# Optimization experiments

Measured on AMD Instinct MI355X. Metric: run time of the kernel, lower is better.

## Reference

```python
import jax, jax.numpy as jnp
import numpy as np

K_DEPTH = 3
JAC_A = 1.0  # alpha (Jacobi a)
JAC_B = 1.0  # beta  (Jacobi b)


def jacobi_filter(sig, gammas):
    """Polynomial graph filter g(sigma) = sum_k gamma_k * P_k^{(a,b)}(sigma),
    Jacobi recurrence applied elementwise (Sigma is diagonal spectrum), domain [-1,1],
    fixed inner scalings (fixI=True => alphas=1)."""
    a, b = JAC_A, JAC_B
    xs = [jnp.ones_like(sig)]
    # L = 1
    coef1 = (a - b) / 2.0
    coef2 = (a + b + 2.0) / 2.0
    xs.append(coef1 * xs[0] + coef2 * sig * xs[0])
    for L in range(2, K_DEPTH + 1):
        cl = 2.0 * L * (L + a + b) * (2 * L - 2 + a + b)
        c1 = (2 * L + a + b - 1) * (2 * L + a + b) * (2 * L + a + b - 2)
        c2 = (2 * L + a + b - 1) * (a * a - b * b)
        c3 = 2.0 * (L - 1 + a) * (L - 1 + b) * (2 * L + a + b)
        xs.append((c1 / cl) * sig * xs[-1] - (c2 / cl) * xs[-1] - (c3 / cl) * xs[-2])
    basis = jnp.stack(xs, axis=0)  # [K+1, B, H, L, d]
    return jnp.einsum('k,kbhld->bhld', gammas, basis)


def setup_inputs() -> dict:
    key = jax.random.key(0)
    ks = jax.random.split(key, 7)
    B, L, Ha, Hs, d = 4, 2048, 4, 4, 64
    mk = lambda k, H: jax.random.normal(k, (B, L, H, d), dtype=jnp.float32)
    return {
        'U': mk(ks[0], Ha),
        'Sigma': mk(ks[1], Ha),
        'V': mk(ks[2], Ha),
        'values': mk(ks[3], Ha),
        'queries_softmax': mk(ks[4], Hs),
        'keys_softmax': mk(ks[5], Hs),
        'values_softmax': mk(ks[6], Hs),
        'gammas': jnp.ones((K_DEPTH + 1,), dtype=jnp.float32),
    }


def reference(U, Sigma, V, values, queries_softmax, keys_softmax, values_softmax, gammas):
    d_k = U.shape[-1]
    # ---- AGF (SVD) heads ----
    Uh = jax.nn.softmax(jnp.transpose(U, (0, 2, 1, 3)), axis=-1)        # [B,H,L,d]
    Vt = jax.nn.softmax(jnp.transpose(V, (0, 2, 3, 1)), axis=-1)        # [B,H,d,L]
    vals = jnp.transpose(values, (0, 2, 1, 3))                           # [B,H,L,d]
    sig = jax.nn.sigmoid(jnp.transpose(Sigma, (0, 2, 1, 3)))             # [B,H,L,d]
    gf = jacobi_filter(sig, gammas)                                       # [B,H,L,d]
    kv = jnp.einsum('bhdl,bhle->bhde', Vt, vals)                          # [B,H,d,d]
    out_agf = jnp.einsum('bhld,bhde->bhle', Uh * gf, kv)                  # [B,H,L,d]
    out_agf = jnp.transpose(out_agf, (0, 2, 1, 3))                        # [B,L,H,d]
    # ---- orthogonality loss ----
    eye = jnp.eye(d_k, dtype=Uh.dtype)
    sym_u = jnp.einsum('bhld,bhle->bhde', Uh, Uh) - eye
    sym_v = jnp.einsum('bhdl,bhel->bhde', Vt, Vt) - eye
    ortho_loss = jnp.mean(jnp.abs(sym_u), axis=(1, 2, 3)) + jnp.mean(jnp.abs(sym_v), axis=(1, 2, 3))
    # ---- softmax (flash) heads ----
    q = jnp.transpose(queries_softmax, (0, 2, 1, 3))
    k = jnp.transpose(keys_softmax, (0, 2, 1, 3))
    v = jnp.transpose(values_softmax, (0, 2, 1, 3))
    scores = jnp.einsum('bhld,bhsd->bhls', q, k) / jnp.sqrt(jnp.asarray(d_k, q.dtype))
    attn = jax.nn.softmax(scores, axis=-1)
    out_sm = jnp.einsum('bhls,bhsd->bhld', attn, v)
    out_sm = jnp.transpose(out_sm, (0, 2, 1, 3))                          # [B,L,H,d]
    out = jnp.concatenate([out_agf, out_sm], axis=2)                      # [B,L,2H,d]
    return out, ortho_loss
```

## Files before the change

### kernel.cpp

```cpp
#include <hip/hip_runtime.h>
#include <hip/hip_bf16.h>

#define BB 4
#define SEQ 2048
#define NH 4
#define D 64
#define NPAIR 16
#define HOUT 8
#define LOSS_BASE ((size_t)BB * SEQ * HOUT * D)

#define N_PART   (4 * 16 * 3 * 4096)
#define OFF_SPART N_PART
#define N_SPART  (16 * 32 * 64)
#define OFF_LPART (OFF_SPART + N_SPART)
#define N_LPART  (2 * 16 * 2048)
#define OFF_F32_END (OFF_LPART + N_LPART)
#define USZ ((size_t)16 * 2048 * 64)

typedef __attribute__((ext_vector_type(8))) short bf16x8;
typedef __attribute__((ext_vector_type(4))) float f32x4;
typedef __attribute__((ext_vector_type(8))) unsigned short us8;
typedef __attribute__((ext_vector_type(4))) unsigned short us4;

__device__ __forceinline__ unsigned short f2bf(float x) {
    union { float f; unsigned u; } v; v.f = x;
    unsigned r = v.u + 0x7fffu + ((v.u >> 16) & 1u);
    return (unsigned short)(r >> 16);
}
__device__ __forceinline__ float bf2f(unsigned short u) {
    union { unsigned u; float f; } v; v.u = ((unsigned)u) << 16; return v.f;
}
__device__ __forceinline__ void load16(const float* p, float* v) {
    const float4* q = (const float4*)p;
    float4 a = q[0], b = q[1], c = q[2], d = q[3];
    v[0]=a.x; v[1]=a.y; v[2]=a.z; v[3]=a.w;
    v[4]=b.x; v[5]=b.y; v[6]=b.z; v[7]=b.w;
    v[8]=c.x; v[9]=c.y; v[10]=c.z; v[11]=c.w;
    v[12]=d.x; v[13]=d.y; v[14]=d.z; v[15]=d.w;
}
__device__ __forceinline__ void wr_bf16x16(unsigned short* dst, const float* v) {
    us8 w0, w1;
#pragma unroll
    for (int i = 0; i < 8; i++) { w0[i] = f2bf(v[i]); w1[i] = f2bf(v[8 + i]); }
    *(us8*)dst = w0; *(us8*)(dst + 8) = w1;
}

__global__ __launch_bounds__(256) void prep(const float* __restrict__ U, const float* __restrict__ Sg,
                                            const float* __restrict__ Vagf, const float* __restrict__ vals,
                                            const float* __restrict__ Ksm, const float* __restrict__ Vsm,
                                            const float* __restrict__ gam,
                                            float* __restrict__ ws, unsigned short* __restrict__ usb,
                                            float* __restrict__ out) {
    int lt = blockIdx.x, p = blockIdx.y, stage = blockIdx.z;
    int b = p >> 2, h = p & 3;
    int tid = threadIdx.x;
    int r = tid >> 2;
    int c0 = (tid & 3) * 16;
    __shared__ float T[64][68];
    unsigned short* Khi   = usb;
    unsigned short* VbfT  = usb + USZ;
    unsigned short* UhT   = usb + 2 * USZ;
    unsigned short* EhiT  = usb + 3 * USZ;
    unsigned short* valsT = usb + 4 * USZ;
    unsigned short* Ughi  = usb + 5 * USZ;
    unsigned short* Uglo  = usb + 6 * USZ;
    float* Spart = ws + OFF_SPART;

    const size_t gbase = ((size_t)(b * SEQ + lt * 64 + r) * NH + h) * D + c0;
    const size_t nbase = ((size_t)(p * SEQ + lt * 64 + r)) * 64 + c0;
    const size_t tbase = ((size_t)p * 64 + r) * 2048 + lt * 64 + c0;
    float v[16], e[16];

    if (stage == 0) {
        load16(U + gbase, v);
        float mx = v[0];
#pragma unroll
        for (int k = 1; k < 16; k++) mx = fmaxf(mx, v[k]);
        mx = fmaxf(mx, __shfl_xor(mx, 1));
        mx = fmaxf(mx, __shfl_xor(mx, 2));
        float sm = 0.0f;
#pragma unroll
        for (int k = 0; k < 16; k++) { v[k] = __expf(v[k] - mx); sm += v[k]; }
        sm += __shfl_xor(sm, 1);
        sm += __shfl_xor(sm, 2);
        float inv = 1.0f / sm;
#pragma unroll
        for (int k = 0; k < 16; k++) { v[k] *= inv; T[r][c0 + k] = v[k]; }
        float sg[16];
        load16(Sg + gbase, sg);
        float g0 = gam[0], g1 = gam[1], g2 = gam[2], g3 = gam[3];
        us8 h0, h1, l0, l1;
#pragma unroll
        for (int k = 0; k < 16; k++) {
            float sig = 1.0f / (1.0f + __expf(-sg[k]));
            float x1 = 2.0f * sig;
            float x2 = 1.875f * sig * x1 - 0.75f;
            float x3 = 1.8666666666666667f * sig * x2 - 0.8f * x1;
            float ug = v[k] * (g0 + g1 * x1 + g2 * x2 + g3 * x3);
            unsigned short hh = f2bf(ug);
            unsigned short ll = f2bf(ug - bf2f(hh));
            if (k < 8) { h0[k] = hh; l0[k] = ll; } else { h1[k - 8] = hh; l1[k - 8] = ll; }
        }
        *(us8*)(Ughi + nbase) = h0; *(us8*)(Ughi + nbase + 8) = h1;
        *(us8*)(Uglo + nbase) = l0; *(us8*)(Uglo + nbase + 8) = l1;
        __syncthreads();
#pragma unroll
        for (int k = 0; k < 16; k++) e[k] = T[c0 + k][r];
        wr_bf16x16(UhT + tbase, e);
    } else if (stage == 1) {
        load16(Vagf + gbase, v);
#pragma unroll
        for (int k = 0; k < 16; k++) T[r][c0 + k] = __expf(v[k]);
        __syncthreads();
        float ssum = 0.0f;
#pragma unroll
        for (int k = 0; k < 16; k++) { e[k] = T[c0 + k][r]; ssum += e[k]; }
        ssum += __shfl_xor(ssum, 1);
        ssum += __shfl_xor(ssum, 2);
        if ((tid & 3) == 0) Spart[(p * 32 + lt) * 64 + r] = ssum;
        wr_bf16x16(EhiT + tbase, e);
    } else if (stage == 2) {
        load16(vals + gbase, v);
#pragma unroll
        for (int k = 0; k < 16; k++) T[r][c0 + k] = v[k];
        __syncthreads();
#pragma unroll
        for (int k = 0; k < 16; k++) e[k] = T[c0 + k][r];
        wr_bf16x16(valsT + tbase, e);
    } else if (stage == 3) {
        load16(Vsm + gbase, v);
#pragma unroll
        for (int k = 0; k < 16; k++) T[r][c0 + k] = v[k];
        __syncthreads();
#pragma unroll
        for (int k = 0; k < 16; k++) e[k] = T[c0 + k][r];
        wr_bf16x16(VbfT + tbase, e);
    } else {
        load16(Ksm + gbase, v);
        wr_bf16x16(Khi + nbase, v);
        if (lt == 0 && p == 0 && tid < BB) out[LOSS_BASE + tid] = 0.0f;
    }
}

#define PSTR 72

__global__ __launch_bounds__(256, 2) void mid(const unsigned short* __restrict__ usb,
                                              const float* __restrict__ Q,
                                              float* __restrict__ part,
                                              unsigned short* __restrict__ OpartUS,
                                              float* __restrict__ lpart) {
    __shared__ __align__(16) unsigned char smem[36864];
    const int bid = blockIdx.x;
    const int tid = threadIdx.x;
    const int w = tid >> 6, lane = tid & 63, lm = lane & 15, quad = lane >> 4;

    if (bid >= 64) {
        int fb = bid - 64;
        int qt2 = fb & 15, p = (fb >> 4) & 15, half = fb >> 8;
        int b = p >> 2, h = p & 3;
        const unsigned short* Khi  = usb;
        const unsigned short* VbfT = usb + USZ;
        unsigned short* Kl = (unsigned short*)smem;
        unsigned short* Vl = Kl + 64 * PSTR;
        unsigned short* Ph = Vl + 64 * PSTR;
        const int srow = tid >> 2, sseg = (tid & 3) * 16;

        bf16x8 qhi[2][2], qlo[2][2];
#pragma unroll
        for (int q = 0; q < 2; q++) {
            int row = qt2 * 128 + q * 64 + w * 16 + lm;
            const float* qp = Q + ((size_t)(b * SEQ + row) * NH + h) * D + quad * 8;
#pragma unroll
            for (int ks = 0; ks < 2; ks++) {
                float qq[8];
                float4 a0 = *(const float4*)(qp + ks * 32);
                float4 a1 = *(const float4*)(qp + ks * 32 + 4);
                qq[0]=a0.x; qq[1]=a0.y; qq[2]=a0.z; qq[3]=a0.w;
                qq[4]=a1.x; qq[5]=a1.y; qq[6]=a1.z; qq[7]=a1.w;
#pragma unroll
                for (int j = 0; j < 8; j++) {
                    float xs = qq[j] * 0.125f;
                    unsigned short hi = f2bf(xs);
                    qhi[q][ks][j] = (short)hi;
                    qlo[q][ks][j] = (short)f2bf(xs - bf2f(hi));
                }
            }
        }

        float rsum[2] = {0.f, 0.f};
        f32x4 o[2][4];
#pragma unroll
        for (int q = 0; q < 2; q++)
#pragma unroll
            for (int t = 0; t < 4; t++) o[q][t] = (f32x4){0.f, 0.f, 0.f, 0.f};

        for (int kt = 0; kt < 16; ++kt) {
            __syncthreads();
            {
                size_t kb = ((size_t)(p * SEQ + half * 1024 + kt * 64 + srow)) * 64 + sseg;
                us8 k0 = *(const us8*)(Khi + kb);
                us8 k1 = *(const us8*)(Khi + kb + 8);
                size_t vb = ((size_t)p * 64 + srow) * 2048 + half * 1024 + kt * 64 + sseg;
                us8 v0 = *(const us8*)(VbfT + vb);
                us8 v1 = *(const us8*)(VbfT + vb + 8);
                *(us8*)&Kl[srow * PSTR + sseg] = k0; *(us8*)&Kl[srow * PSTR + sseg + 8] = k1;
                *(us8*)&Vl[srow * PSTR + sseg] = v0; *(us8*)&Vl[srow * PSTR + sseg + 8] = v1;
            }
            __syncthreads();

            bf16x8 kfr[4][2], vfr[4][2];
#pragma unroll
            for (int t = 0; t < 4; t++)
#pragma unroll
                for (int ks = 0; ks < 2; ks++) {
                    kfr[t][ks] = *(const bf16x8*)&Kl[(t * 16 + lm) * PSTR + ks * 32 + quad * 8];
                    vfr[t][ks] = *(const bf16x8*)&Vl[(t * 16 + lm) * PSTR + ks * 32 + quad * 8];
                }

#pragma unroll
            for (int q = 0; q < 2; q++) {
                unsigned short* Phq = Ph + (size_t)(w * 2 + q) * 16 * PSTR;
                f32x4 s[4];
#pragma unroll
                for (int t = 0; t < 4; t++) s[t] = (f32x4){0.f, 0.f, 0.f, 0.f};
#pragma unroll
                for (int t = 0; t < 4; t++)
#pragma unroll
                    for (int ks = 0; ks < 2; ks++) {
                        s[t] = __builtin_amdgcn_mfma_f32_16x16x32_bf16(kfr[t][ks], qhi[q][ks], s[t], 0, 0, 0);
                        s[t] = __builtin_amdgcn_mfma_f32_16x16x32_bf16(kfr[t][ks], qlo[q][ks], s[t], 0, 0, 0);
                    }
#pragma unroll
                for (int t = 0; t < 4; t++) {
                    float e0 = __expf(s[t][0]);
                    float e1 = __expf(s[t][1]);
                    float e2 = __expf(s[t][2]);
                    float e3 = __expf(s[t][3]);
                    rsum[q] += (e0 + e1) + (e2 + e3);
                    us4 pk;
                    pk[0] = f2bf(e0); pk[1] = f2bf(e1); pk[2] = f2bf(e2); pk[3] = f2bf(e3);
                    *(us4*)&Phq[lm * PSTR + t * 16 + quad * 4] = pk;
                }
                bf16x8 pf0 = *(const bf16x8*)&Phq[lm * PSTR + quad * 8];
                bf16x8 pf1 = *(const bf16x8*)&Phq[lm * PSTR + 32 + quad * 8];
#pragma unroll
                for (int dt = 0; dt < 4; dt++) {
                    o[q][dt] = __builtin_amdgcn_mfma_f32_16x16x32_bf16(vfr[dt][0], pf0, o[q][dt], 0, 0, 0);
                    o[q][dt] = __builtin_amdgcn_mfma_f32_16x16x32_bf16(vfr[dt][1], pf1, o[q][dt], 0, 0, 0);
                }
            }
        }

#pragma unroll
        for (int q = 0; q < 2; q++) {
            float rs = rsum[q];
            rs += __shfl_xor(rs, 16);
            rs += __shfl_xor(rs, 32);
            int qrow = qt2 * 128 + q * 64 + w * 16 + lm;
            size_t ob = ((size_t)(half * 16 + p) * SEQ + qrow) * 64;
#pragma unroll
            for (int dt = 0; dt < 4; dt++) {
                us4 pk;
#pragma unroll
                for (int r = 0; r < 4; r++) pk[r] = f2bf(o[q][dt][r]);
                *(us4*)(OpartUS + ob + dt * 16 + quad * 4) = pk;
            }
            if (quad == 0) lpart[(size_t)(half * 16 + p) * SEQ + qrow] = rs;
        }
    } else {
        int split = bid >> 4, p = bid & 15;
        const unsigned short* UhT   = usb + 2 * USZ;
        const unsigned short* EhiT  = usb + 3 * USZ;
        const unsigned short* valsT = usb + 4 * USZ;
        unsigned short* Ut = (unsigned short*)smem;
        unsigned short* Eh = Ut + 64 * 40;
        unsigned short* Vt = Eh + 64 * 40;
        f32x4 su[4], sv[4], kv[4];
#pragma unroll
        for (int i = 0; i < 4; i++) { su[i] = (f32x4){0,0,0,0}; sv[i] = (f32x4){0,0,0,0}; kv[i] = (f32x4){0,0,0,0}; }
        int srow = tid >> 2;
        int sseg = (tid & 3) * 8;

        for (int step = 0; step < 16; ++step) {
            int l0 = split * 512 + step * 32;
            __syncthreads();
            size_t gb = ((size_t)p * 64 + srow) * 2048 + l0 + sseg;
            *(us8*)&Ut[srow * 40 + sseg] = *(const us8*)(UhT + gb);
            *(us8*)&Eh[srow * 40 + sseg] = *(const us8*)(EhiT + gb);
            *(us8*)&Vt[srow * 40 + sseg] = *(const us8*)(valsT + gb);
            __syncthreads();
            int ao = (w * 16 + lm) * 40 + quad * 8;
            bf16x8 au  = *(const bf16x8*)&Ut[ao];
            bf16x8 aeh = *(const bf16x8*)&Eh[ao];
#pragma unroll
            for (int nt = 0; nt < 4; nt++) {
                int bo = (nt * 16 + lm) * 40 + quad * 8;
                bf16x8 bu  = *(const bf16x8*)&Ut[bo];
                bf16x8 beh = *(const bf16x8*)&Eh[bo];
                bf16x8 bv  = *(const bf16x8*)&Vt[bo];
                su[nt] = __builtin_amdgcn_mfma_f32_16x16x32_bf16(au,  bu,  su[nt], 0, 0, 0);
                sv[nt] = __builtin_amdgcn_mfma_f32_16x16x32_bf16(aeh, beh, sv[nt], 0, 0, 0);
                kv[nt] = __builtin_amdgcn_mfma_f32_16x16x32_bf16(aeh, bv,  kv[nt], 0, 0, 0);
            }
        }
        float* dst = part + (size_t)(split * 16 + p) * 3 * 4096;
#pragma unroll
        for (int nt = 0; nt < 4; nt++)
#pragma unroll
            for (int reg = 0; reg < 4; reg++) {
                int off = (w * 16 + quad * 4 + reg) * 64 + nt * 16 + lm;
                dst[off] = su[nt][reg];
                dst[4096 + off] = sv[nt][reg];
                dst[8192 + off] = kv[nt][reg];
            }
    }
}

__global__ __launch_bounds__(256) void post(const float* __restrict__ part, const float* __restrict__ Spart,
                                            const unsigned short* __restrict__ usb,
                                            const unsigned short* __restrict__ OpartUS,
                                            const float* __restrict__ lpart, float* __restrict__ out) {
    const int bid = blockIdx.x;
    const int tid = threadIdx.x;
    if (bid < 2048) {
        int idx = bid * 256 + tid;
        int p = idx >> 15;
        int rem = idx & 32767;
        int l = rem >> 4, dq = rem & 15;
        int b = p >> 2, h = p & 3;
        us4 a = *(const us4*)(OpartUS + ((size_t)p * SEQ + l) * 64 + dq * 4);
        us4 c = *(const us4*)(OpartUS + ((size_t)(16 + p) * SEQ + l) * 64 + dq * 4);
        float inv = 1.0f / (lpart[(size_t)p * SEQ + l] + lpart[(size_t)(16 + p) * SEQ + l]);
        f32x4 res;
#pragma unroll
        for (int r = 0; r < 4; r++) res[r] = (bf2f(a[r]) + bf2f(c[r])) * inv;
        *(f32x4*)(out + ((size_t)(b * SEQ + l) * HOUT + 4 + h) * D + dq * 4) = res;
        return;
    }
    const int w = tid >> 6, lane = tid & 63, lm = lane & 15, quad = lane >> 4;
    int j = bid - 2048;
    int p = (j < 512) ? (j >> 5) : (j - 512);
    __shared__ float cis[64];
    __shared__ float red[4][64];
    __shared__ __align__(16) unsigned short KVh[64 * PSTR];
    __shared__ __align__(16) unsigned short KVl[64 * PSTR];
    {
        int d = tid & 63, grp = tid >> 6;
        float s = 0.0f;
#pragma unroll
        for (int i = 0; i < 8; i++) s += Spart[(p * 32 + grp * 8 + i) * 64 + d];
        red[grp][d] = s;
        __syncthreads();
        if (tid < 64) cis[tid] = 1.0f / (red[0][tid] + red[1][tid] + red[2][tid] + red[3][tid]);
        __syncthreads();
    }
    if (j >= 512) {
        float s = 0.0f;
        for (int idx = tid; idx < 8192; idx += 256) {
            int g = idx >> 12, i = idx & 4095;
            float v = 0.0f;
#pragma unroll
            for (int sp = 0; sp < 4; sp++) v += part[((size_t)(sp * 16 + p) * 3 + g) * 4096 + i];
            if (g) v *= cis[i >> 6] * cis[i & 63];
            float dg = ((i >> 6) == (i & 63)) ? 1.0f : 0.0f;
            s += fabsf(v - dg);
        }
#pragma unroll
        for (int o = 32; o > 0; o >>= 1) s += __shfl_xor(s, o);
        if ((tid & 63) == 0) red[0][(tid >> 6) * 2] = s;
        __syncthreads();
        if (tid == 0)
            atomicAdd(&out[LOSS_BASE + (p >> 2)],
                      (red[0][0] + red[0][2] + red[0][4] + red[0][6]) * (1.0f / 16384.0f));
        return;
    }
    int lt = j & 31;
    int b = p >> 2, h = p & 3;
    const unsigned short* Ughi = usb + 5 * USZ;
    const unsigned short* Uglo = usb + 6 * USZ;
    for (int idx = tid; idx < 4096; idx += 256) {
        int d = idx >> 6, e = idx & 63;
        float v = 0.0f;
#pragma unroll
        for (int sp = 0; sp < 4; sp++) v += part[((size_t)(sp * 16 + p) * 3 + 2) * 4096 + idx];
        v *= cis[d];
        unsigned short hh = f2bf(v);
        KVh[e * PSTR + d] = hh;
        KVl[e * PSTR + d] = f2bf(v - bf2f(hh));
    }
    __syncthreads();
    size_t ub = ((size_t)(p * SEQ + lt * 64 + w * 16 + lm)) * 64 + quad * 8;
    bf16x8 ah[2], al[2];
#pragma unroll
    for (int ks = 0; ks < 2; ks++) {
        ah[ks] = *(const bf16x8*)(Ughi + ub + ks * 32);
        al[ks] = *(const bf16x8*)(Uglo + ub + ks * 32);
    }
    f32x4 acc[4];
#pragma unroll
    for (int nt = 0; nt < 4; nt++) acc[nt] = (f32x4){0.f, 0.f, 0.f, 0.f};
#pragma unroll
    for (int nt = 0; nt < 4; nt++)
#pragma unroll
        for (int ks = 0; ks < 2; ks++) {
            bf16x8 bh = *(const bf16x8*)&KVh[(nt * 16 + lm) * PSTR + ks * 32 + quad * 8];
            bf16x8 bl = *(const bf16x8*)&KVl[(nt * 16 + lm) * PSTR + ks * 32 + quad * 8];
            acc[nt] = __builtin_amdgcn_mfma_f32_16x16x32_bf16(ah[ks], bh, acc[nt], 0, 0, 0);
            acc[nt] = __builtin_amdgcn_mfma_f32_16x16x32_bf16(al[ks], bh, acc[nt], 0, 0, 0);
            acc[nt] = __builtin_amdgcn_mfma_f32_16x16x32_bf16(ah[ks], bl, acc[nt], 0, 0, 0);
        }
#pragma unroll
    for (int nt = 0; nt < 4; nt++)
#pragma unroll
        for (int reg = 0; reg < 4; reg++)
            out[((size_t)(b * SEQ + lt * 64 + w * 16 + quad * 4 + reg) * HOUT + h) * D + nt * 16 + lm] =
                acc[nt][reg];
}

extern "C" void kernel_launch(void* const* d_in, const int* in_sizes, int n_in,
                              void* d_out, int out_size, void* d_ws, size_t ws_size,
                              hipStream_t stream) {
    (void)in_sizes; (void)n_in; (void)out_size; (void)ws_size;
    const float* U    = (const float*)d_in[0];
    const float* Sg   = (const float*)d_in[1];
    const float* V    = (const float*)d_in[2];
    const float* vals = (const float*)d_in[3];
    const float* Qs   = (const float*)d_in[4];
    const float* Ks   = (const float*)d_in[5];
    const float* Vv   = (const float*)d_in[6];
    const float* gam  = (const float*)d_in[7];
    float* out = (float*)d_out;

    float* ws = (float*)d_ws;
    float* part  = ws;
    float* Spart = ws + OFF_SPART;
    float* lpart = ws + OFF_LPART;
    unsigned short* usb = (unsigned short*)(ws + OFF_F32_END);
    unsigned short* OpartUS = usb + 7 * USZ;

    prep<<<dim3(32, 16, 5), 256, 0, stream>>>(U, Sg, V, vals, Ks, Vv, gam, ws, usb, out);
    mid<<<576, 256, 0, stream>>>(usb, Qs, part, OpartUS, lpart);
    post<<<2576, 256, 0, stream>>>(part, Spart, usb, OpartUS, lpart, out);
}
```

Baseline: 165.7 us.

## Split softmax attention keys four ways and use packed bf16 conversion with exp2

```diff
diff --git a/kernel.cpp b/kernel.cpp
--- a/kernel.cpp
+++ b/kernel.cpp
@@ -13,7 +13,7 @@
 #define OFF_SPART N_PART
 #define N_SPART  (16 * 32 * 64)
 #define OFF_LPART (OFF_SPART + N_SPART)
-#define N_LPART  (2 * 16 * 2048)
+#define N_LPART  (4 * 16 * 2048)
 #define OFF_F32_END (OFF_LPART + N_LPART)
 #define USZ ((size_t)16 * 2048 * 64)
 
@@ -29,6 +29,11 @@
 }
 __device__ __forceinline__ float bf2f(unsigned short u) {
     union { unsigned u; float f; } v; v.u = ((unsigned)u) << 16; return v.f;
+}
+__device__ __forceinline__ unsigned cvt_pk_bf16(float lo, float hi) {
+    unsigned r;
+    asm("v_cvt_pk_bf16_f32 %0, %1, %2" : "=v"(r) : "v"(lo), "v"(hi));
+    return r;
 }
 __device__ __forceinline__ void load16(const float* p, float* v) {
     const float4* q = (const float4*)p;
@@ -39,10 +44,11 @@
     v[12]=d.x; v[13]=d.y; v[14]=d.z; v[15]=d.w;
 }
 __device__ __forceinline__ void wr_bf16x16(unsigned short* dst, const float* v) {
-    us8 w0, w1;
-#pragma unroll
-    for (int i = 0; i < 8; i++) { w0[i] = f2bf(v[i]); w1[i] = f2bf(v[8 + i]); }
-    *(us8*)dst = w0; *(us8*)(dst + 8) = w1;
+    unsigned w[8];
+#pragma unroll
+    for (int i = 0; i < 8; i++) w[i] = cvt_pk_bf16(v[2 * i], v[2 * i + 1]);
+    *(uint4*)dst = make_uint4(w[0], w[1], w[2], w[3]);
+    *(uint4*)(dst + 8) = make_uint4(w[4], w[5], w[6], w[7]);
 }
 
 __global__ __launch_bounds__(256) void prep(const float* __restrict__ U, const float* __restrict__ Sg,
@@ -143,8 +149,9 @@
 }
 
 #define PSTR 72
-
-__global__ __launch_bounds__(256, 2) void mid(const unsigned short* __restrict__ usb,
+#define QSC 0.18033688011112042f
+
+__global__ __launch_bounds__(256, 4) void mid(const unsigned short* __restrict__ usb,
                                               const float* __restrict__ Q,
                                               float* __restrict__ part,
                                               unsigned short* __restrict__ OpartUS,
@@ -156,7 +163,7 @@
 
     if (bid >= 64) {
         int fb = bid - 64;
-        int qt2 = fb & 15, p = (fb >> 4) & 15, half = fb >> 8;
+        int qt2 = fb & 15, p = (fb >> 4) & 15, qr = fb >> 8;
         int b = p >> 2, h = p & 3;
         const unsigned short* Khi  = usb;
         const unsigned short* VbfT = usb + USZ;
@@ -179,7 +186,7 @@
                 qq[4]=a1.x; qq[5]=a1.y; qq[6]=a1.z; qq[7]=a1.w;
 #pragma unroll
                 for (int j = 0; j < 8; j++) {
-                    float xs = qq[j] * 0.125f;
+                    float xs = qq[j] * QSC;
                     unsigned short hi = f2bf(xs);
                     qhi[q][ks][j] = (short)hi;
                     qlo[q][ks][j] = (short)f2bf(xs - bf2f(hi));
@@ -194,13 +201,13 @@
 #pragma unroll
             for (int t = 0; t < 4; t++) o[q][t] = (f32x4){0.f, 0.f, 0.f, 0.f};
 
-        for (int kt = 0; kt < 16; ++kt) {
+        for (int kt = 0; kt < 8; ++kt) {
             __syncthreads();
             {
-                size_t kb = ((size_t)(p * SEQ + half * 1024 + kt * 64 + srow)) * 64 + sseg;
+                size_t kb = ((size_t)(p * SEQ + qr * 512 + kt * 64 + srow)) * 64 + sseg;
                 us8 k0 = *(const us8*)(Khi + kb);
                 us8 k1 = *(const us8*)(Khi + kb + 8);
-                size_t vb = ((size_t)p * 64 + srow) * 2048 + half * 1024 + kt * 64 + sseg;
+                size_t vb = ((size_t)p * 64 + srow) * 2048 + qr * 512 + kt * 64 + sseg;
                 us8 v0 = *(const us8*)(VbfT + vb);
                 us8 v1 = *(const us8*)(VbfT + vb + 8);
                 *(us8*)&Kl[srow * PSTR + sseg] = k0; *(us8*)&Kl[srow * PSTR + sseg + 8] = k1;
@@ -232,14 +239,14 @@
                     }
 #pragma unroll
                 for (int t = 0; t < 4; t++) {
-                    float e0 = __expf(s[t][0]);
-                    float e1 = __expf(s[t][1]);
-                    float e2 = __expf(s[t][2]);
-                    float e3 = __expf(s[t][3]);
+                    float e0 = exp2f(s[t][0]);
+                    float e1 = exp2f(s[t][1]);
+                    float e2 = exp2f(s[t][2]);
+                    float e3 = exp2f(s[t][3]);
                     rsum[q] += (e0 + e1) + (e2 + e3);
-                    us4 pk;
-                    pk[0] = f2bf(e0); pk[1] = f2bf(e1); pk[2] = f2bf(e2); pk[3] = f2bf(e3);
-                    *(us4*)&Phq[lm * PSTR + t * 16 + quad * 4] = pk;
+                    unsigned w0 = cvt_pk_bf16(e0, e1);
+                    unsigned w1 = cvt_pk_bf16(e2, e3);
+                    *(uint2*)&Phq[lm * PSTR + t * 16 + quad * 4] = make_uint2(w0, w1);
                 }
                 bf16x8 pf0 = *(const bf16x8*)&Phq[lm * PSTR + quad * 8];
                 bf16x8 pf1 = *(const bf16x8*)&Phq[lm * PSTR + 32 + quad * 8];
@@ -257,15 +264,14 @@
             rs += __shfl_xor(rs, 16);
             rs += __shfl_xor(rs, 32);
             int qrow = qt2 * 128 + q * 64 + w * 16 + lm;
-            size_t ob = ((size_t)(half * 16 + p) * SEQ + qrow) * 64;
+            size_t ob = ((size_t)(qr * 16 + p) * SEQ + qrow) * 64;
 #pragma unroll
             for (int dt = 0; dt < 4; dt++) {
-                us4 pk;
-#pragma unroll
-                for (int r = 0; r < 4; r++) pk[r] = f2bf(o[q][dt][r]);
-                *(us4*)(OpartUS + ob + dt * 16 + quad * 4) = pk;
-            }
-            if (quad == 0) lpart[(size_t)(half * 16 + p) * SEQ + qrow] = rs;
+                unsigned w0 = cvt_pk_bf16(o[q][dt][0], o[q][dt][1]);
+                unsigned w1 = cvt_pk_bf16(o[q][dt][2], o[q][dt][3]);
+                *(uint2*)(OpartUS + ob + dt * 16 + quad * 4) = make_uint2(w0, w1);
+            }
+            if (quad == 0) lpart[(size_t)(qr * 16 + p) * SEQ + qrow] = rs;
         }
     } else {
         int split = bid >> 4, p = bid & 15;
@@ -328,12 +334,18 @@
         int rem = idx & 32767;
         int l = rem >> 4, dq = rem & 15;
         int b = p >> 2, h = p & 3;
-        us4 a = *(const us4*)(OpartUS + ((size_t)p * SEQ + l) * 64 + dq * 4);
-        us4 c = *(const us4*)(OpartUS + ((size_t)(16 + p) * SEQ + l) * 64 + dq * 4);
-        float inv = 1.0f / (lpart[(size_t)p * SEQ + l] + lpart[(size_t)(16 + p) * SEQ + l]);
-        f32x4 res;
-#pragma unroll
-        for (int r = 0; r < 4; r++) res[r] = (bf2f(a[r]) + bf2f(c[r])) * inv;
+        f32x4 res = (f32x4){0.f, 0.f, 0.f, 0.f};
+        float lsum = 0.0f;
+#pragma unroll
+        for (int qr = 0; qr < 4; qr++) {
+            us4 a = *(const us4*)(OpartUS + ((size_t)(qr * 16 + p) * SEQ + l) * 64 + dq * 4);
+            lsum += lpart[(size_t)(qr * 16 + p) * SEQ + l];
+#pragma unroll
+            for (int r = 0; r < 4; r++) res[r] += bf2f(a[r]);
+        }
+        float inv = 1.0f / lsum;
+#pragma unroll
+        for (int r = 0; r < 4; r++) res[r] *= inv;
         *(f32x4*)(out + ((size_t)(b * SEQ + l) * HOUT + 4 + h) * D + dq * 4) = res;
         return;
     }
@@ -439,6 +451,6 @@
     unsigned short* OpartUS = usb + 7 * USZ;
 
     prep<<<dim3(32, 16, 5), 256, 0, stream>>>(U, Sg, V, vals, Ks, Vv, gam, ws, usb, out);
-    mid<<<576, 256, 0, stream>>>(usb, Qs, part, OpartUS, lpart);
+    mid<<<1088, 256, 0, stream>>>(usb, Qs, part, OpartUS, lpart);
     post<<<2576, 256, 0, stream>>>(part, Spart, usb, OpartUS, lpart, out);
 }
```

Result: slower. 227.9 us (+37.6%).
